# Performance work log

Hardware: AMD Instinct MI355X
Metric: run time of the kernel (lower is better)

Reference implementation:

```python
import jax, jax.numpy as jnp
import numpy as np

N_NODES = 100000
N_EDGES = 1600000
IN_D = 128
H_D = 128
OUT_D = 128
N_GRAPHS = 64


def _linear_params(key, fan_in, fan_out):
    k1, k2 = jax.random.split(key)
    bound = 1.0 / np.sqrt(fan_in)
    w = jax.random.uniform(k1, (fan_in, fan_out), jnp.float32, -bound, bound)
    b = jax.random.uniform(k2, (fan_out,), jnp.float32, -bound, bound)
    return w, b


def setup_inputs() -> dict:
    key = jax.random.key(0)
    ks = jax.random.split(key, 16)
    x = jax.random.normal(ks[0], (N_NODES, IN_D), jnp.float32)
    edge_index = jax.random.randint(ks[1], (2, N_EDGES), 0, N_NODES, jnp.int64)
    batch = jnp.sort(jax.random.randint(ks[2], (N_NODES,), 0, N_GRAPHS, jnp.int64))
    w1_1, b1_1 = _linear_params(ks[3], IN_D, H_D)
    w2_1, b2_1 = _linear_params(ks[4], H_D, H_D)
    w1_2, b1_2 = _linear_params(ks[5], H_D, H_D)
    w2_2, b2_2 = _linear_params(ks[6], H_D, H_D)
    w1_3, b1_3 = _linear_params(ks[7], H_D, H_D)
    w2_3, b2_3 = _linear_params(ks[8], H_D, OUT_D)
    return {
        "x": x, "edge_index": edge_index, "batch": batch,
        "w1_1": w1_1, "b1_1": b1_1, "w2_1": w2_1, "b2_1": b2_1,
        "w1_2": w1_2, "b1_2": b1_2, "w2_2": w2_2, "b2_2": b2_2,
        "w1_3": w1_3, "b1_3": b1_3, "w2_3": w2_3, "b2_3": b2_3,
    }


def _gin_conv(x, src, dst, w1, b1, w2, b2):
    # sum-aggregate source features onto destination nodes, eps=0 -> add self
    agg = jax.ops.segment_sum(x[src], dst, num_segments=N_NODES)
    h = agg + x
    # MLP: Linear -> ReLU -> Linear
    h = jnp.maximum(h @ w1 + b1, 0.0) @ w2 + b2
    return h


def reference(x, edge_index, batch,
              w1_1, b1_1, w2_1, b2_1,
              w1_2, b1_2, w2_2, b2_2,
              w1_3, b1_3, w2_3, b2_3):
    src, dst = edge_index[0], edge_index[1]
    h = jax.nn.relu(_gin_conv(x, src, dst, w1_1, b1_1, w2_1, b2_1))
    h = jax.nn.relu(_gin_conv(h, src, dst, w1_2, b1_2, w2_2, b2_2))
    h = _gin_conv(h, src, dst, w1_3, b1_3, w2_3, b2_3)
    # global mean pool over graphs, then flatten
    sums = jax.ops.segment_sum(h, batch, num_segments=N_GRAPHS)
    counts = jax.ops.segment_sum(jnp.ones((h.shape[0],), h.dtype), batch, num_segments=N_GRAPHS)
    pooled = sums / jnp.maximum(counts, 1.0)[:, None]
    return pooled.reshape(-1)
```

## Files before the change

kernel.cpp:

```cpp
#include <hip/hip_runtime.h>

#define D 128
#define NB_E 512

typedef __attribute__((ext_vector_type(8))) short bf16x8;
typedef __attribute__((ext_vector_type(16))) float f32x16;

__device__ inline float b2f(unsigned int hi16_as_lo) {
  union { unsigned int u; float f; } v;
  v.u = hi16_as_lo;
  return v.f;
}
__device__ inline unsigned short f2b(float f) {
  union { float f; unsigned int u; } v;
  v.f = f;
  unsigned int r = v.u + 0x7FFFu + ((v.u >> 16) & 1u);
  return (unsigned short)(r >> 16);
}
__device__ inline unsigned int pk2(float lo, float hi) {
  return (unsigned int)f2b(lo) | ((unsigned int)f2b(hi) << 16);
}

__global__ __launch_bounds__(256) void convert_kernel(
    const float* __restrict__ in, unsigned short* __restrict__ out, int n8) {
  int i = blockIdx.x * 256 + threadIdx.x;
  if (i >= n8) return;
  const float4 a = *reinterpret_cast<const float4*>(in + (size_t)i * 8);
  const float4 b = *reinterpret_cast<const float4*>(in + (size_t)i * 8 + 4);
  unsigned short o[8] = {f2b(a.x), f2b(a.y), f2b(a.z), f2b(a.w),
                         f2b(b.x), f2b(b.y), f2b(b.z), f2b(b.w)};
  *reinterpret_cast<bf16x8*>(out + (size_t)i * 8) =
      *reinterpret_cast<bf16x8*>(o);
}

__global__ __launch_bounds__(256) void pack_w6_kernel(
    const float* __restrict__ w0, const float* __restrict__ w1,
    const float* __restrict__ w2, const float* __restrict__ w3,
    const float* __restrict__ w4, const float* __restrict__ w5,
    unsigned short* __restrict__ Wp) {
  const int m = blockIdx.x >> 3;
  const float* W = m == 0 ? w0
                 : m == 1 ? w1
                 : m == 2 ? w2
                 : m == 3 ? w3
                 : m == 4 ? w4
                          : w5;
  const int idx = (blockIdx.x & 7) * 256 + threadIdx.x;
  const int l = idx & 63;
  const int s = (idx >> 6) & 7;
  const int t = idx >> 9;
  const int n = (t << 5) + (l & 31);
  const int k0 = (s << 4) + ((l >> 5) << 3);
  unsigned short o[8];
#pragma unroll
  for (int i = 0; i < 8; ++i) o[i] = f2b(W[(size_t)(k0 + i) * D + n]);
  *reinterpret_cast<bf16x8*>(Wp + (size_t)m * 16384 + (size_t)idx * 8) =
      *reinterpret_cast<bf16x8*>(o);
}

__global__ __launch_bounds__(256) void bktA_kernel(
    const int* __restrict__ dst, int* __restrict__ bcount, int n_edges,
    int NBU, int epb) {
  __shared__ int cnt[512];
  for (int i = threadIdx.x; i < NBU; i += 256) cnt[i] = 0;
  __syncthreads();
  const int e0 = blockIdx.x * epb;
  const int e1 = min(e0 + epb, n_edges);
  for (int e = e0 + threadIdx.x; e < e1; e += 256)
    atomicAdd(&cnt[dst[e] >> 8], 1);
  __syncthreads();
  int* out = bcount + (size_t)blockIdx.x * NBU;
  for (int i = threadIdx.x; i < NBU; i += 256) out[i] = cnt[i];
}

__global__ __launch_bounds__(256) void bktB_kernel(
    const int* __restrict__ bcount, int* __restrict__ boff,
    int* __restrict__ btot, int NBU) {
  __shared__ int lds[256];
  const int j = blockIdx.x;
  const int t = threadIdx.x;
  const int a = bcount[(size_t)(2 * t) * NBU + j];
  const int b = bcount[(size_t)(2 * t + 1) * NBU + j];
  const int s = a + b;
  lds[t] = s;
  __syncthreads();
#pragma unroll
  for (int off = 1; off < 256; off <<= 1) {
    int p = 0;
    if (t >= off) p = lds[t - off];
    __syncthreads();
    lds[t] += p;
    __syncthreads();
  }
  const int excl = lds[t] - s;
  boff[(size_t)(2 * t) * NBU + j] = excl;
  boff[(size_t)(2 * t + 1) * NBU + j] = excl + a;
  if (t == 255) btot[j] = lds[255];
}

__global__ __launch_bounds__(256) void bktBase_kernel(
    const int* __restrict__ btot, int* __restrict__ base, int NBU) {
  __shared__ int lds[256];
  const int t = threadIdx.x;
  const int a = (2 * t < NBU) ? btot[2 * t] : 0;
  const int b = (2 * t + 1 < NBU) ? btot[2 * t + 1] : 0;
  const int s = a + b;
  lds[t] = s;
  __syncthreads();
#pragma unroll
  for (int off = 1; off < 256; off <<= 1) {
    int p = 0;
    if (t >= off) p = lds[t - off];
    __syncthreads();
    lds[t] += p;
    __syncthreads();
  }
  const int excl = lds[t] - s;
  if (2 * t <= NBU) base[2 * t] = excl;
  if (2 * t + 1 <= NBU) base[2 * t + 1] = excl + a;
}

__global__ __launch_bounds__(256) void bktC_kernel(
    const int* __restrict__ src, const int* __restrict__ dst,
    const int* __restrict__ boff, const int* __restrict__ base,
    unsigned int* __restrict__ ebuf, int n_edges, int NBU, int epb) {
  __shared__ int cur[512];
  const int* bo = boff + (size_t)blockIdx.x * NBU;
  for (int i = threadIdx.x; i < NBU; i += 256) cur[i] = base[i] + bo[i];
  __syncthreads();
  const int e0 = blockIdx.x * epb;
  const int e1 = min(e0 + epb, n_edges);
  for (int e = e0 + threadIdx.x; e < e1; e += 256) {
    const int d = dst[e];
    const int pos = atomicAdd(&cur[d >> 8], 1);
    ebuf[pos] = ((unsigned int)(d & 255) << 17) | (unsigned int)src[e];
  }
}

__global__ __launch_bounds__(256) void bktD_kernel(
    const unsigned int* __restrict__ ebuf, const int* __restrict__ base,
    int* __restrict__ rowptr, int* __restrict__ col, int n_nodes) {
  __shared__ int hist[256];
  __shared__ int lds[256];
  __shared__ int cursor[256];
  const int j = blockIdx.x;
  const int t = threadIdx.x;
  hist[t] = 0;
  __syncthreads();
  const int e0 = base[j], e1 = base[j + 1];
  for (int e = e0 + t; e < e1; e += 256)
    atomicAdd(&hist[ebuf[e] >> 17], 1);
  __syncthreads();
  const int h = hist[t];
  lds[t] = h;
  __syncthreads();
#pragma unroll
  for (int off = 1; off < 256; off <<= 1) {
    int p = 0;
    if (t >= off) p = lds[t - off];
    __syncthreads();
    lds[t] += p;
    __syncthreads();
  }
  const int excl = lds[t] - h;
  const int node = (j << 8) + t;
  if (node <= n_nodes) rowptr[node] = e0 + excl;
  cursor[t] = e0 + excl;
  __syncthreads();
  for (int e = e0 + t; e < e1; e += 256) {
    const unsigned int v = ebuf[e];
    const int pos = atomicAdd(&cursor[v >> 17], 1);
    col[pos] = (int)(v & 0x1FFFFu);
  }
}

__global__ __launch_bounds__(256) void gather_bf16_kernel(
    const unsigned short* __restrict__ X, const int* __restrict__ rowptr,
    const int* __restrict__ col, unsigned short* __restrict__ out,
    int n_nodes) {
  const int t = blockIdx.x * 256 + threadIdx.x;
  const int g = t >> 5;
  if (g >= n_nodes) return;
  const int c = t & 15;
  const int slot = (t >> 4) & 1;
  const uint4* Xv = reinterpret_cast<const uint4*>(X);
  float a0 = 0.f, a1 = 0.f, a2 = 0.f, a3 = 0.f;
  float a4 = 0.f, a5 = 0.f, a6 = 0.f, a7 = 0.f;
  if (slot == 0) {
    const uint4 u = Xv[(size_t)g * 16 + c];
    a0 = b2f(u.x << 16); a1 = b2f(u.x & 0xffff0000u);
    a2 = b2f(u.y << 16); a3 = b2f(u.y & 0xffff0000u);
    a4 = b2f(u.z << 16); a5 = b2f(u.z & 0xffff0000u);
    a6 = b2f(u.w << 16); a7 = b2f(u.w & 0xffff0000u);
  }
  const int beg = rowptr[g], end = rowptr[g + 1];
  int j = beg + slot;
  for (; j + 6 < end; j += 8) {
    const int s0 = col[j + 0];
    const int s1 = col[j + 2];
    const int s2 = col[j + 4];
    const int s3 = col[j + 6];
    const uint4 w0 = Xv[(size_t)s0 * 16 + c];
    const uint4 w1 = Xv[(size_t)s1 * 16 + c];
    const uint4 w2 = Xv[(size_t)s2 * 16 + c];
    const uint4 w3 = Xv[(size_t)s3 * 16 + c];
    a0 += b2f(w0.x << 16); a1 += b2f(w0.x & 0xffff0000u);
    a2 += b2f(w0.y << 16); a3 += b2f(w0.y & 0xffff0000u);
    a4 += b2f(w0.z << 16); a5 += b2f(w0.z & 0xffff0000u);
    a6 += b2f(w0.w << 16); a7 += b2f(w0.w & 0xffff0000u);
    a0 += b2f(w1.x << 16); a1 += b2f(w1.x & 0xffff0000u);
    a2 += b2f(w1.y << 16); a3 += b2f(w1.y & 0xffff0000u);
    a4 += b2f(w1.z << 16); a5 += b2f(w1.z & 0xffff0000u);
    a6 += b2f(w1.w << 16); a7 += b2f(w1.w & 0xffff0000u);
    a0 += b2f(w2.x << 16); a1 += b2f(w2.x & 0xffff0000u);
    a2 += b2f(w2.y << 16); a3 += b2f(w2.y & 0xffff0000u);
    a4 += b2f(w2.z << 16); a5 += b2f(w2.z & 0xffff0000u);
    a6 += b2f(w2.w << 16); a7 += b2f(w2.w & 0xffff0000u);
    a0 += b2f(w3.x << 16); a1 += b2f(w3.x & 0xffff0000u);
    a2 += b2f(w3.y << 16); a3 += b2f(w3.y & 0xffff0000u);
    a4 += b2f(w3.z << 16); a5 += b2f(w3.z & 0xffff0000u);
    a6 += b2f(w3.w << 16); a7 += b2f(w3.w & 0xffff0000u);
  }
  for (; j < end; j += 2) {
    const uint4 w = Xv[(size_t)col[j] * 16 + c];
    a0 += b2f(w.x << 16); a1 += b2f(w.x & 0xffff0000u);
    a2 += b2f(w.y << 16); a3 += b2f(w.y & 0xffff0000u);
    a4 += b2f(w.z << 16); a5 += b2f(w.z & 0xffff0000u);
    a6 += b2f(w.w << 16); a7 += b2f(w.w & 0xffff0000u);
  }
  a0 += __shfl_xor(a0, 16, 64);
  a1 += __shfl_xor(a1, 16, 64);
  a2 += __shfl_xor(a2, 16, 64);
  a3 += __shfl_xor(a3, 16, 64);
  a4 += __shfl_xor(a4, 16, 64);
  a5 += __shfl_xor(a5, 16, 64);
  a6 += __shfl_xor(a6, 16, 64);
  a7 += __shfl_xor(a7, 16, 64);
  if (slot == 0) {
    uint4 o;
    o.x = pk2(a0, a1);
    o.y = pk2(a2, a3);
    o.z = pk2(a4, a5);
    o.w = pk2(a6, a7);
    reinterpret_cast<uint4*>(out)[(size_t)g * 16 + c] = o;
  }
}

template <int RELU>
__global__ __launch_bounds__(512) void mlp2_kernel(
    const unsigned short* __restrict__ X, const unsigned short* __restrict__ Wp1,
    const unsigned short* __restrict__ Wp2, const float* __restrict__ bias1,
    const float* __restrict__ bias2, unsigned short* __restrict__ out,
    int n_strips) {
  __shared__ unsigned short wl1[16384];
  __shared__ unsigned short wl2[16384];
  __shared__ float bl1[128], bl2[128];

  const int lx = threadIdx.x & 63;
  const int wid = threadIdx.x >> 6;
  const int strip = blockIdx.x * 8 + wid;
  const int h = lx >> 5;
  const int nl = lx & 31;

  bf16x8 xf[8];
  if (strip < n_strips) {
    const unsigned short* xrow = X + (size_t)(strip * 32 + nl) * D + h * 8;
#pragma unroll
    for (int s = 0; s < 8; ++s)
      xf[s] = *reinterpret_cast<const bf16x8*>(xrow + s * 16);
  }

  for (int i = threadIdx.x * 8; i < 16384; i += 512 * 8) {
    *reinterpret_cast<bf16x8*>(wl1 + i) = *reinterpret_cast<const bf16x8*>(Wp1 + i);
    *reinterpret_cast<bf16x8*>(wl2 + i) = *reinterpret_cast<const bf16x8*>(Wp2 + i);
  }
  if (threadIdx.x < 128) {
    bl1[threadIdx.x] = bias1[threadIdx.x];
    bl2[threadIdx.x] = bias2[threadIdx.x];
  }
  __syncthreads();
  if (strip >= n_strips) return;

  f32x16 acc1[4];
#pragma unroll
  for (int t1 = 0; t1 < 4; ++t1)
#pragma unroll
    for (int r = 0; r < 16; ++r)
      acc1[t1][r] = bl1[32 * t1 + (r & 3) + 8 * (r >> 2) + 4 * h];
#pragma unroll
  for (int s = 0; s < 8; ++s) {
#pragma unroll
    for (int t1 = 0; t1 < 4; ++t1) {
      const bf16x8 wf = *reinterpret_cast<const bf16x8*>(
          wl1 + ((t1 * 8 + s) * 64 + lx) * 8);
      acc1[t1] =
          __builtin_amdgcn_mfma_f32_32x32x16_bf16(wf, xf[s], acc1[t1], 0, 0, 0);
    }
  }

  f32x16 acc2[4];
#pragma unroll
  for (int t = 0; t < 4; ++t)
#pragma unroll
    for (int r = 0; r < 16; ++r)
      acc2[t][r] = bl2[32 * t + (r & 3) + 8 * (r >> 2) + 4 * h];
#pragma unroll
  for (int s2 = 0; s2 < 8; ++s2) {
    const int t1 = s2 >> 1;
    const int ro = (s2 & 1) << 3;
    const float g0 = fmaxf(acc1[t1][ro + 0], 0.f);
    const float g1 = fmaxf(acc1[t1][ro + 1], 0.f);
    const float g2 = fmaxf(acc1[t1][ro + 2], 0.f);
    const float g3 = fmaxf(acc1[t1][ro + 3], 0.f);
    const float g4 = fmaxf(acc1[t1][ro + 4], 0.f);
    const float g5 = fmaxf(acc1[t1][ro + 5], 0.f);
    const float g6 = fmaxf(acc1[t1][ro + 6], 0.f);
    const float g7 = fmaxf(acc1[t1][ro + 7], 0.f);
    const unsigned int pA0 = pk2(g0, g1), pA1 = pk2(g2, g3);
    const unsigned int pB0 = pk2(g4, g5), pB1 = pk2(g6, g7);
    const unsigned int sA0 = (unsigned int)__shfl((int)pA0, lx ^ 32, 64);
    const unsigned int sA1 = (unsigned int)__shfl((int)pA1, lx ^ 32, 64);
    const unsigned int sB0 = (unsigned int)__shfl((int)pB0, lx ^ 32, 64);
    const unsigned int sB1 = (unsigned int)__shfl((int)pB1, lx ^ 32, 64);
    union { unsigned int u[4]; bf16x8 v; } fr;
    fr.u[0] = h ? sB0 : pA0;
    fr.u[1] = h ? sB1 : pA1;
    fr.u[2] = h ? pB0 : sA0;
    fr.u[3] = h ? pB1 : sA1;
#pragma unroll
    for (int t = 0; t < 4; ++t) {
      const bf16x8 wf = *reinterpret_cast<const bf16x8*>(
          wl2 + ((t * 8 + s2) * 64 + lx) * 8);
      acc2[t] =
          __builtin_amdgcn_mfma_f32_32x32x16_bf16(wf, fr.v, acc2[t], 0, 0, 0);
    }
  }

  unsigned short* orow = out + (size_t)(strip * 32 + nl) * D + h * 8;
#pragma unroll
  for (int s = 0; s < 8; ++s) {
    const int t = s >> 1;
    const int ro = (s & 1) << 3;
    float g0 = acc2[t][ro + 0], g1 = acc2[t][ro + 1];
    float g2 = acc2[t][ro + 2], g3 = acc2[t][ro + 3];
    float g4 = acc2[t][ro + 4], g5 = acc2[t][ro + 5];
    float g6 = acc2[t][ro + 6], g7 = acc2[t][ro + 7];
    if (RELU) {
      g0 = fmaxf(g0, 0.f); g1 = fmaxf(g1, 0.f);
      g2 = fmaxf(g2, 0.f); g3 = fmaxf(g3, 0.f);
      g4 = fmaxf(g4, 0.f); g5 = fmaxf(g5, 0.f);
      g6 = fmaxf(g6, 0.f); g7 = fmaxf(g7, 0.f);
    }
    const unsigned int pA0 = pk2(g0, g1), pA1 = pk2(g2, g3);
    const unsigned int pB0 = pk2(g4, g5), pB1 = pk2(g6, g7);
    const unsigned int sA0 = (unsigned int)__shfl((int)pA0, lx ^ 32, 64);
    const unsigned int sA1 = (unsigned int)__shfl((int)pA1, lx ^ 32, 64);
    const unsigned int sB0 = (unsigned int)__shfl((int)pB0, lx ^ 32, 64);
    const unsigned int sB1 = (unsigned int)__shfl((int)pB1, lx ^ 32, 64);
    union { unsigned int u[4]; bf16x8 v; } fr;
    fr.u[0] = h ? sB0 : pA0;
    fr.u[1] = h ? sB1 : pA1;
    fr.u[2] = h ? pB0 : sA0;
    fr.u[3] = h ? pB1 : sA1;
    *reinterpret_cast<bf16x8*>(orow + s * 16) = fr.v;
  }
}

#define POOL_NODES_PER_GROUP 128

__global__ __launch_bounds__(256) void pool_kernel(
    const unsigned short* __restrict__ H, const int* __restrict__ batch,
    float* __restrict__ sums, float* __restrict__ counts, int n_nodes) {
  const int group = (blockIdx.x * 256 + threadIdx.x) >> 5;
  const int lane = threadIdx.x & 31;
  const int n0 = group * POOL_NODES_PER_GROUP;
  if (n0 >= n_nodes) return;
  const int n1 = min(n0 + POOL_NODES_PER_GROUP, n_nodes);
  const uint2* Hv = reinterpret_cast<const uint2*>(H);

  float a0 = 0.f, a1 = 0.f, a2 = 0.f, a3 = 0.f;
  int cur = batch[n0];
  int runlen = 0;
  for (int n = n0; n < n1; ++n) {
    const int g = batch[n];
    if (g != cur) {
      float* p = sums + (size_t)cur * D + lane * 4;
      unsafeAtomicAdd(p + 0, a0);
      unsafeAtomicAdd(p + 1, a1);
      unsafeAtomicAdd(p + 2, a2);
      unsafeAtomicAdd(p + 3, a3);
      if (lane == 0) unsafeAtomicAdd(counts + cur, (float)runlen);
      a0 = a1 = a2 = a3 = 0.f;
      cur = g;
      runlen = 0;
    }
    const uint2 v = Hv[(size_t)n * 32 + lane];
    a0 += b2f(v.x << 16);
    a1 += b2f(v.x & 0xffff0000u);
    a2 += b2f(v.y << 16);
    a3 += b2f(v.y & 0xffff0000u);
    ++runlen;
  }
  float* p = sums + (size_t)cur * D + lane * 4;
  unsafeAtomicAdd(p + 0, a0);
  unsafeAtomicAdd(p + 1, a1);
  unsafeAtomicAdd(p + 2, a2);
  unsafeAtomicAdd(p + 3, a3);
  if (lane == 0) unsafeAtomicAdd(counts + cur, (float)runlen);
}

__global__ __launch_bounds__(256) void pool_norm_kernel(
    float* __restrict__ out, const float* __restrict__ counts, int n) {
  int i = blockIdx.x * 256 + threadIdx.x;
  if (i >= n) return;
  float cnt = counts[i / D];
  out[i] = out[i] / fmaxf(cnt, 1.0f);
}

extern "C" void kernel_launch(void* const* d_in, const int* in_sizes, int n_in,
                              void* d_out, int out_size, void* d_ws,
                              size_t ws_size, hipStream_t stream) {
  const float* x = (const float*)d_in[0];
  const int* ei = (const int*)d_in[1];
  const int* batch = (const int*)d_in[2];
  const float* B[6] = {(const float*)d_in[4],  (const float*)d_in[6],
                       (const float*)d_in[8],  (const float*)d_in[10],
                       (const float*)d_in[12], (const float*)d_in[14]};

  const int n_nodes = in_sizes[2];
  const int n_edges = in_sizes[1] / 2;
  const int n_graphs = out_size / D;
  const int* src = ei;
  const int* dst = ei + n_edges;

  const size_t matB = (size_t)n_nodes * D * sizeof(unsigned short);
  unsigned short* bufA = (unsigned short*)d_ws;
  unsigned short* bufB = (unsigned short*)((char*)d_ws + matB);
  unsigned short* bufC = (unsigned short*)((char*)d_ws + 2 * matB);
  unsigned short* wpack = (unsigned short*)((char*)d_ws + 3 * matB);
  int* rowptr = (int*)((char*)wpack + 6 * 16384 * sizeof(unsigned short));
  int* colidx = rowptr + (n_nodes + 1);
  unsigned int* ebuf = (unsigned int*)(colidx + n_edges);
  const int NBU = (n_nodes + 255) >> 8;
  int* bcount = (int*)(ebuf + n_edges);
  int* boff = bcount + (size_t)NB_E * NBU;
  int* btot = boff + (size_t)NB_E * NBU;
  int* base = btot + NBU;
  float* counts = (float*)(base + NBU + 2);

  const dim3 blk(256);
  const int gather_blocks = (int)(((long long)n_nodes * 32 + 255) / 256);
  const int pool_groups =
      (n_nodes + POOL_NODES_PER_GROUP - 1) / POOL_NODES_PER_GROUP;
  const int pool_blocks = (pool_groups * 32 + 255) / 256;
  const int n_strips = n_nodes / 32;
  const int mlp_grid = (n_strips + 7) / 8;
  const int epb = (n_edges + NB_E - 1) / NB_E;

  convert_kernel<<<(n_nodes * (D / 8) + 255) / 256, blk, 0, stream>>>(
      x, bufA, n_nodes * (D / 8));
  pack_w6_kernel<<<48, blk, 0, stream>>>(
      (const float*)d_in[3], (const float*)d_in[5], (const float*)d_in[7],
      (const float*)d_in[9], (const float*)d_in[11], (const float*)d_in[13],
      wpack);

  bktA_kernel<<<NB_E, blk, 0, stream>>>(dst, bcount, n_edges, NBU, epb);
  bktB_kernel<<<NBU, blk, 0, stream>>>(bcount, boff, btot, NBU);
  bktBase_kernel<<<1, blk, 0, stream>>>(btot, base, NBU);
  bktC_kernel<<<NB_E, blk, 0, stream>>>(src, dst, boff, base, ebuf, n_edges,
                                        NBU, epb);
  bktD_kernel<<<NBU, blk, 0, stream>>>(ebuf, base, rowptr, colidx, n_nodes);

  gather_bf16_kernel<<<gather_blocks, blk, 0, stream>>>(bufA, rowptr, colidx,
                                                        bufB, n_nodes);
  mlp2_kernel<1><<<mlp_grid, 512, 0, stream>>>(bufB, wpack + 0 * 16384,
                                               wpack + 1 * 16384, B[0], B[1],
                                               bufC, n_strips);
  gather_bf16_kernel<<<gather_blocks, blk, 0, stream>>>(bufC, rowptr, colidx,
                                                        bufB, n_nodes);
  mlp2_kernel<1><<<mlp_grid, 512, 0, stream>>>(bufB, wpack + 2 * 16384,
                                               wpack + 3 * 16384, B[2], B[3],
                                               bufA, n_strips);
  gather_bf16_kernel<<<gather_blocks, blk, 0, stream>>>(bufA, rowptr, colidx,
                                                        bufB, n_nodes);
  mlp2_kernel<0><<<mlp_grid, 512, 0, stream>>>(bufB, wpack + 4 * 16384,
                                               wpack + 5 * 16384, B[4], B[5],
                                               bufC, n_strips);

  hipMemsetAsync(d_out, 0, (size_t)out_size * sizeof(float), stream);
  hipMemsetAsync(counts, 0, (size_t)n_graphs * sizeof(float), stream);
  pool_kernel<<<pool_blocks, blk, 0, stream>>>(bufC, batch, (float*)d_out,
                                               counts, n_nodes);
  pool_norm_kernel<<<(out_size + 255) / 256, blk, 0, stream>>>((float*)d_out,
                                                               counts,
                                                               out_size);
}
```

Before: 357.0 us.

## Make MLP kernel persistent with prefetched strips and amortized weight staging

The fused two-layer MLP kernel now launches a fixed grid of 512 blocks of 256 threads. Each wave processes a contiguous range of 32-row strips instead of exactly one. The 64 KB of bf16 weights staged into shared memory is loaded once per block and reused across many strips, and the next strip's input fragment is prefetched into registers while the current strip is computed. This trades extra register pressure from the double-buffered inputs and lower occupancy for fewer redundant weight loads and better latency hiding.

```diff
diff --git a/kernel.cpp b/kernel.cpp
--- a/kernel.cpp
+++ b/kernel.cpp
@@ -247,7 +247,7 @@
 }
 
 template <int RELU>
-__global__ __launch_bounds__(512) void mlp2_kernel(
+__global__ __launch_bounds__(256) void mlp2_kernel(
     const unsigned short* __restrict__ X, const unsigned short* __restrict__ Wp1,
     const unsigned short* __restrict__ Wp2, const float* __restrict__ bias1,
     const float* __restrict__ bias2, unsigned short* __restrict__ out,
@@ -258,19 +258,22 @@
 
   const int lx = threadIdx.x & 63;
   const int wid = threadIdx.x >> 6;
-  const int strip = blockIdx.x * 8 + wid;
   const int h = lx >> 5;
   const int nl = lx & 31;
-
-  bf16x8 xf[8];
-  if (strip < n_strips) {
-    const unsigned short* xrow = X + (size_t)(strip * 32 + nl) * D + h * 8;
-#pragma unroll
-    for (int s = 0; s < 8; ++s)
-      xf[s] = *reinterpret_cast<const bf16x8*>(xrow + s * 16);
-  }
-
-  for (int i = threadIdx.x * 8; i < 16384; i += 512 * 8) {
+  const int wg = blockIdx.x * 4 + wid;
+  const int NW = gridDim.x * 4;
+  int s = (int)(((long long)wg * n_strips) / NW);
+  const int s_end = (int)(((long long)(wg + 1) * n_strips) / NW);
+
+  bf16x8 xfA[8], xfB[8];
+  if (s < s_end) {
+    const unsigned short* xrow = X + (size_t)(s * 32 + nl) * D + h * 8;
+#pragma unroll
+    for (int k = 0; k < 8; ++k)
+      xfA[k] = *reinterpret_cast<const bf16x8*>(xrow + k * 16);
+  }
+
+  for (int i = threadIdx.x * 8; i < 16384; i += 256 * 8) {
     *reinterpret_cast<bf16x8*>(wl1 + i) = *reinterpret_cast<const bf16x8*>(Wp1 + i);
     *reinterpret_cast<bf16x8*>(wl2 + i) = *reinterpret_cast<const bf16x8*>(Wp2 + i);
   }
@@ -279,90 +282,101 @@
     bl2[threadIdx.x] = bias2[threadIdx.x];
   }
   __syncthreads();
-  if (strip >= n_strips) return;
-
-  f32x16 acc1[4];
-#pragma unroll
-  for (int t1 = 0; t1 < 4; ++t1)
-#pragma unroll
-    for (int r = 0; r < 16; ++r)
-      acc1[t1][r] = bl1[32 * t1 + (r & 3) + 8 * (r >> 2) + 4 * h];
-#pragma unroll
-  for (int s = 0; s < 8; ++s) {
-#pragma unroll
-    for (int t1 = 0; t1 < 4; ++t1) {
-      const bf16x8 wf = *reinterpret_cast<const bf16x8*>(
-          wl1 + ((t1 * 8 + s) * 64 + lx) * 8);
-      acc1[t1] =
-          __builtin_amdgcn_mfma_f32_32x32x16_bf16(wf, xf[s], acc1[t1], 0, 0, 0);
+
+  for (; s < s_end; ++s) {
+    if (s + 1 < s_end) {
+      const unsigned short* xrow = X + (size_t)((s + 1) * 32 + nl) * D + h * 8;
+#pragma unroll
+      for (int k = 0; k < 8; ++k)
+        xfB[k] = *reinterpret_cast<const bf16x8*>(xrow + k * 16);
     }
-  }
-
-  f32x16 acc2[4];
-#pragma unroll
-  for (int t = 0; t < 4; ++t)
-#pragma unroll
-    for (int r = 0; r < 16; ++r)
-      acc2[t][r] = bl2[32 * t + (r & 3) + 8 * (r >> 2) + 4 * h];
-#pragma unroll
-  for (int s2 = 0; s2 < 8; ++s2) {
-    const int t1 = s2 >> 1;
-    const int ro = (s2 & 1) << 3;
-    const float g0 = fmaxf(acc1[t1][ro + 0], 0.f);
-    const float g1 = fmaxf(acc1[t1][ro + 1], 0.f);
-    const float g2 = fmaxf(acc1[t1][ro + 2], 0.f);
-    const float g3 = fmaxf(acc1[t1][ro + 3], 0.f);
-    const float g4 = fmaxf(acc1[t1][ro + 4], 0.f);
-    const float g5 = fmaxf(acc1[t1][ro + 5], 0.f);
-    const float g6 = fmaxf(acc1[t1][ro + 6], 0.f);
-    const float g7 = fmaxf(acc1[t1][ro + 7], 0.f);
-    const unsigned int pA0 = pk2(g0, g1), pA1 = pk2(g2, g3);
-    const unsigned int pB0 = pk2(g4, g5), pB1 = pk2(g6, g7);
-    const unsigned int sA0 = (unsigned int)__shfl((int)pA0, lx ^ 32, 64);
-    const unsigned int sA1 = (unsigned int)__shfl((int)pA1, lx ^ 32, 64);
-    const unsigned int sB0 = (unsigned int)__shfl((int)pB0, lx ^ 32, 64);
-    const unsigned int sB1 = (unsigned int)__shfl((int)pB1, lx ^ 32, 64);
-    union { unsigned int u[4]; bf16x8 v; } fr;
-    fr.u[0] = h ? sB0 : pA0;
-    fr.u[1] = h ? sB1 : pA1;
-    fr.u[2] = h ? pB0 : sA0;
-    fr.u[3] = h ? pB1 : sA1;
-#pragma unroll
-    for (int t = 0; t < 4; ++t) {
-      const bf16x8 wf = *reinterpret_cast<const bf16x8*>(
-          wl2 + ((t * 8 + s2) * 64 + lx) * 8);
-      acc2[t] =
-          __builtin_amdgcn_mfma_f32_32x32x16_bf16(wf, fr.v, acc2[t], 0, 0, 0);
+
+    f32x16 acc1[4];
+#pragma unroll
+    for (int t1 = 0; t1 < 4; ++t1)
+#pragma unroll
+      for (int r = 0; r < 16; ++r)
+        acc1[t1][r] = bl1[32 * t1 + (r & 3) + 8 * (r >> 2) + 4 * h];
+#pragma unroll
+    for (int k = 0; k < 8; ++k) {
+#pragma unroll
+      for (int t1 = 0; t1 < 4; ++t1) {
+        const bf16x8 wf = *reinterpret_cast<const bf16x8*>(
+            wl1 + ((t1 * 8 + k) * 64 + lx) * 8);
+        acc1[t1] = __builtin_amdgcn_mfma_f32_32x32x16_bf16(wf, xfA[k], acc1[t1],
+                                                           0, 0, 0);
+      }
     }
-  }
-
-  unsigned short* orow = out + (size_t)(strip * 32 + nl) * D + h * 8;
-#pragma unroll
-  for (int s = 0; s < 8; ++s) {
-    const int t = s >> 1;
-    const int ro = (s & 1) << 3;
-    float g0 = acc2[t][ro + 0], g1 = acc2[t][ro + 1];
-    float g2 = acc2[t][ro + 2], g3 = acc2[t][ro + 3];
-    float g4 = acc2[t][ro + 4], g5 = acc2[t][ro + 5];
-    float g6 = acc2[t][ro + 6], g7 = acc2[t][ro + 7];
-    if (RELU) {
-      g0 = fmaxf(g0, 0.f); g1 = fmaxf(g1, 0.f);
-      g2 = fmaxf(g2, 0.f); g3 = fmaxf(g3, 0.f);
-      g4 = fmaxf(g4, 0.f); g5 = fmaxf(g5, 0.f);
-      g6 = fmaxf(g6, 0.f); g7 = fmaxf(g7, 0.f);
+
+    f32x16 acc2[4];
+#pragma unroll
+    for (int t = 0; t < 4; ++t)
+#pragma unroll
+      for (int r = 0; r < 16; ++r)
+        acc2[t][r] = bl2[32 * t + (r & 3) + 8 * (r >> 2) + 4 * h];
+#pragma unroll
+    for (int s2 = 0; s2 < 8; ++s2) {
+      const int t1 = s2 >> 1;
+      const int ro = (s2 & 1) << 3;
+      const float g0 = fmaxf(acc1[t1][ro + 0], 0.f);
+      const float g1 = fmaxf(acc1[t1][ro + 1], 0.f);
+      const float g2 = fmaxf(acc1[t1][ro + 2], 0.f);
+      const float g3 = fmaxf(acc1[t1][ro + 3], 0.f);
+      const float g4 = fmaxf(acc1[t1][ro + 4], 0.f);
+      const float g5 = fmaxf(acc1[t1][ro + 5], 0.f);
+      const float g6 = fmaxf(acc1[t1][ro + 6], 0.f);
+      const float g7 = fmaxf(acc1[t1][ro + 7], 0.f);
+      const unsigned int pA0 = pk2(g0, g1), pA1 = pk2(g2, g3);
+      const unsigned int pB0 = pk2(g4, g5), pB1 = pk2(g6, g7);
+      const unsigned int sA0 = (unsigned int)__shfl((int)pA0, lx ^ 32, 64);
+      const unsigned int sA1 = (unsigned int)__shfl((int)pA1, lx ^ 32, 64);
+      const unsigned int sB0 = (unsigned int)__shfl((int)pB0, lx ^ 32, 64);
+      const unsigned int sB1 = (unsigned int)__shfl((int)pB1, lx ^ 32, 64);
+      union { unsigned int u[4]; bf16x8 v; } fr;
+      fr.u[0] = h ? sB0 : pA0;
+      fr.u[1] = h ? sB1 : pA1;
+      fr.u[2] = h ? pB0 : sA0;
+      fr.u[3] = h ? pB1 : sA1;
+#pragma unroll
+      for (int t = 0; t < 4; ++t) {
+        const bf16x8 wf = *reinterpret_cast<const bf16x8*>(
+            wl2 + ((t * 8 + s2) * 64 + lx) * 8);
+        acc2[t] = __builtin_amdgcn_mfma_f32_32x32x16_bf16(wf, fr.v, acc2[t],
+                                                          0, 0, 0);
+      }
     }
-    const unsigned int pA0 = pk2(g0, g1), pA1 = pk2(g2, g3);
-    const unsigned int pB0 = pk2(g4, g5), pB1 = pk2(g6, g7);
-    const unsigned int sA0 = (unsigned int)__shfl((int)pA0, lx ^ 32, 64);
-    const unsigned int sA1 = (unsigned int)__shfl((int)pA1, lx ^ 32, 64);
-    const unsigned int sB0 = (unsigned int)__shfl((int)pB0, lx ^ 32, 64);
-    const unsigned int sB1 = (unsigned int)__shfl((int)pB1, lx ^ 32, 64);
-    union { unsigned int u[4]; bf16x8 v; } fr;
-    fr.u[0] = h ? sB0 : pA0;
-    fr.u[1] = h ? sB1 : pA1;
-    fr.u[2] = h ? pB0 : sA0;
-    fr.u[3] = h ? pB1 : sA1;
-    *reinterpret_cast<bf16x8*>(orow + s * 16) = fr.v;
+
+    unsigned short* orow = out + (size_t)(s * 32 + nl) * D + h * 8;
+#pragma unroll
+    for (int k = 0; k < 8; ++k) {
+      const int t = k >> 1;
+      const int ro = (k & 1) << 3;
+      float g0 = acc2[t][ro + 0], g1 = acc2[t][ro + 1];
+      float g2 = acc2[t][ro + 2], g3 = acc2[t][ro + 3];
+      float g4 = acc2[t][ro + 4], g5 = acc2[t][ro + 5];
+      float g6 = acc2[t][ro + 6], g7 = acc2[t][ro + 7];
+      if (RELU) {
+        g0 = fmaxf(g0, 0.f); g1 = fmaxf(g1, 0.f);
+        g2 = fmaxf(g2, 0.f); g3 = fmaxf(g3, 0.f);
+        g4 = fmaxf(g4, 0.f); g5 = fmaxf(g5, 0.f);
+        g6 = fmaxf(g6, 0.f); g7 = fmaxf(g7, 0.f);
+      }
+      const unsigned int pA0 = pk2(g0, g1), pA1 = pk2(g2, g3);
+      const unsigned int pB0 = pk2(g4, g5), pB1 = pk2(g6, g7);
+      const unsigned int sA0 = (unsigned int)__shfl((int)pA0, lx ^ 32, 64);
+      const unsigned int sA1 = (unsigned int)__shfl((int)pA1, lx ^ 32, 64);
+      const unsigned int sB0 = (unsigned int)__shfl((int)pB0, lx ^ 32, 64);
+      const unsigned int sB1 = (unsigned int)__shfl((int)pB1, lx ^ 32, 64);
+      union { unsigned int u[4]; bf16x8 v; } fr;
+      fr.u[0] = h ? sB0 : pA0;
+      fr.u[1] = h ? sB1 : pA1;
+      fr.u[2] = h ? pB0 : sA0;
+      fr.u[3] = h ? pB1 : sA1;
+      *reinterpret_cast<bf16x8*>(orow + k * 16) = fr.v;
+    }
+
+#pragma unroll
+    for (int k = 0; k < 8; ++k) xfA[k] = xfB[k];
   }
 }
 
@@ -454,7 +468,7 @@
       (n_nodes + POOL_NODES_PER_GROUP - 1) / POOL_NODES_PER_GROUP;
   const int pool_blocks = (pool_groups * 32 + 255) / 256;
   const int n_strips = n_nodes / 32;
-  const int mlp_grid = (n_strips + 7) / 8;
+  const int mlp_grid = 512;
   const int epb = (n_edges + NB_E - 1) / NB_E;
 
   convert_kernel<<<(n_nodes * (D / 8) + 255) / 256, blk, 0, stream>>>(
@@ -473,17 +487,17 @@
 
   gather_bf16_kernel<<<gather_blocks, blk, 0, stream>>>(bufA, rowptr, colidx,
                                                         bufB, n_nodes);
-  mlp2_kernel<1><<<mlp_grid, 512, 0, stream>>>(bufB, wpack + 0 * 16384,
+  mlp2_kernel<1><<<mlp_grid, blk, 0, stream>>>(bufB, wpack + 0 * 16384,
                                                wpack + 1 * 16384, B[0], B[1],
                                                bufC, n_strips);
   gather_bf16_kernel<<<gather_blocks, blk, 0, stream>>>(bufC, rowptr, colidx,
                                                         bufB, n_nodes);
-  mlp2_kernel<1><<<mlp_grid, 512, 0, stream>>>(bufB, wpack + 2 * 16384,
+  mlp2_kernel<1><<<mlp_grid, blk, 0, stream>>>(bufB, wpack + 2 * 16384,
                                                wpack + 3 * 16384, B[2], B[3],
                                                bufA, n_strips);
   gather_bf16_kernel<<<gather_blocks, blk, 0, stream>>>(bufA, rowptr, colidx,
                                                         bufB, n_nodes);
-  mlp2_kernel<0><<<mlp_grid, 512, 0, stream>>>(bufB, wpack + 4 * 16384,
+  mlp2_kernel<0><<<mlp_grid, blk, 0, stream>>>(bufB, wpack + 4 * 16384,
                                                wpack + 5 * 16384, B[4], B[5],
                                                bufC, n_strips);
 
```

After: 407.3 us. 14.1% more time.
